# Kernel optimization log

Measured on AMD Instinct MI355X. Metric: run time of the kernel, lower is better.

Reference implementation:

```python
import jax, jax.numpy as jnp
import numpy as np

IN_FEATURES = 4096
OUT_FEATURES = 4096
M_TOKENS = 8192
WEIGHT_SCALE = 0.1
OUT_SCALE = 0.1


def setup_inputs() -> dict:
    key = jax.random.key(0)
    k_x, k_w = jax.random.split(key)
    # int8-valued activations and weights in [-128, 128), stored as int32 carriers
    x_q = jax.random.randint(k_x, (M_TOKENS, IN_FEATURES), 0, 256, dtype=jnp.int32) - 128
    weight_q = jax.random.randint(k_w, (OUT_FEATURES, IN_FEATURES), 0, 256, dtype=jnp.int32) - 128
    scale_x = jnp.float32(0.05)
    return {"x_q": x_q, "weight_q": weight_q, "scale_x": scale_x}


def reference(x_q, weight_q, scale_x):
    acc = jnp.einsum("mk,nk->mn", x_q.astype(jnp.int32), weight_q.astype(jnp.int32))
    # fused epilogue: rescale, round-to-nearest, saturate to int8
    scale = scale_x * jnp.float32(WEIGHT_SCALE) / jnp.float32(OUT_SCALE)
    y = acc.astype(jnp.float32) * scale
    y_q = jnp.clip(jnp.round(y), -128.0, 127.0).astype(jnp.int8)
    return (y_q, jnp.float32(OUT_SCALE))
```

## Files before the change

kernel.cpp:

```cpp
#include <hip/hip_runtime.h>
#include <stdint.h>

typedef int v4i  __attribute__((ext_vector_type(4)));
typedef int v16i __attribute__((ext_vector_type(16)));

#define M_TOK 8192
#define N_OUT 4096
#define K_IN  4096

__device__ __forceinline__ int pack4(int4 a) {
    return (a.x & 255) | ((a.y & 255) << 8) | ((a.z & 255) << 16) | ((a.w & 255) << 24);
}

__global__ __launch_bounds__(256) void pack_both(
    const int4* __restrict__ x, const int4* __restrict__ w,
    int* __restrict__ dA, int* __restrict__ dB, int n4x, int n4w)
{
    int i = blockIdx.x * blockDim.x + threadIdx.x;
    if (i < n4x) {
        dA[i] = pack4(x[i]);
    } else {
        int j = i - n4x;
        if (j < n4w) dB[j] = pack4(w[j]);
    }
}

__global__ __launch_bounds__(256) void gemm_i8_kernel(
    const char* __restrict__ A8,
    const char* __restrict__ B8,
    const float* __restrict__ scale_ptr,
    float* __restrict__ out)
{
    __shared__ alignas(16) char lA[128 * 128];
    __shared__ alignas(16) char lB[128 * 128];

    const int tid  = threadIdx.x;
    const int wave = tid >> 6;
    const int lane = tid & 63;

    const int bm = blockIdx.y * 128;
    const int bn = blockIdx.x * 128;

    const int wm = (wave >> 1) * 64;
    const int wn = (wave & 1) * 64;

    v16i acc[2][2];
#pragma unroll
    for (int i = 0; i < 2; ++i)
#pragma unroll
        for (int j = 0; j < 2; ++j)
#pragma unroll
            for (int r = 0; r < 16; ++r)
                acc[i][j][r] = 0;

    const int srow = lane >> 3;
    const int scol = ((lane & 7) ^ srow) << 4;

    const char* gA[4]; const char* gB[4];
    char* lAp[4]; char* lBp[4];
#pragma unroll
    for (int q = 0; q < 4; ++q) {
        int row0 = wave * 32 + q * 8;
        gA[q] = A8 + (size_t)(bm + row0 + srow) * K_IN + scol;
        gB[q] = B8 + (size_t)(bn + row0 + srow) * K_IN + scol;
        lAp[q] = lA + row0 * 128;
        lBp[q] = lB + row0 * 128;
    }

    const int fm = lane & 31;
    const int fh = lane >> 5;
    const int fsw = fm & 7;

    for (int k0 = 0; k0 < K_IN; k0 += 128) {
#pragma unroll
        for (int q = 0; q < 4; ++q) {
            __builtin_amdgcn_global_load_lds(
                (const __attribute__((address_space(1))) void*)(gA[q] + k0),
                (__attribute__((address_space(3))) void*)lAp[q], 16, 0, 0);
            __builtin_amdgcn_global_load_lds(
                (const __attribute__((address_space(1))) void*)(gB[q] + k0),
                (__attribute__((address_space(3))) void*)lBp[q], 16, 0, 0);
        }

        __syncthreads();

#pragma unroll
        for (int kk = 0; kk < 4; ++kk) {
            const int goff = ((kk * 2 + fh) ^ fsw) << 4;
            v4i af[2], bf[2];
#pragma unroll
            for (int t = 0; t < 2; ++t) {
                af[t] = *(const v4i*)(lA + (wm + t * 32 + fm) * 128 + goff);
                bf[t] = *(const v4i*)(lB + (wn + t * 32 + fm) * 128 + goff);
            }
#pragma unroll
            for (int ti = 0; ti < 2; ++ti)
#pragma unroll
                for (int tj = 0; tj < 2; ++tj)
                    acc[ti][tj] = __builtin_amdgcn_mfma_i32_32x32x32_i8(
                        af[ti], bf[tj], acc[ti][tj], 0, 0, 0);
        }

        __syncthreads();
    }

    const float s     = scale_ptr[0];
    const float scale = (s * 0.1f) / 0.1f;

#pragma unroll
    for (int ti = 0; ti < 2; ++ti) {
#pragma unroll
        for (int tj = 0; tj < 2; ++tj) {
#pragma unroll
            for (int r = 0; r < 16; ++r) {
                int row = bm + wm + ti * 32 + (r & 3) + 8 * (r >> 2) + 4 * fh;
                int col = bn + wn + tj * 32 + fm;
                float y = (float)acc[ti][tj][r] * scale;
                y = rintf(y);
                y = fminf(fmaxf(y, -128.0f), 127.0f);
                out[(size_t)row * N_OUT + col] = y;
            }
        }
    }

    if (bm == 0 && bn == 0 && tid == 0)
        out[(size_t)M_TOK * N_OUT] = 0.1f;
}

extern "C" void kernel_launch(void* const* d_in, const int* in_sizes, int n_in,
                              void* d_out, int out_size, void* d_ws, size_t ws_size,
                              hipStream_t stream)
{
    const int*   x_q     = (const int*)d_in[0];
    const int*   w_q     = (const int*)d_in[1];
    const float* scale_x = (const float*)d_in[2];
    float* out = (float*)d_out;

    char* A8 = (char*)d_ws;
    char* B8 = (char*)d_ws + (size_t)M_TOK * K_IN;

    const int n4x = (M_TOK * K_IN) / 4;
    const int n4w = (N_OUT * K_IN) / 4;

    pack_both<<<(n4x + n4w) / 256, 256, 0, stream>>>(
        (const int4*)x_q, (const int4*)w_q, (int*)A8, (int*)B8, n4x, n4w);

    dim3 grid(N_OUT / 128, M_TOK / 128);
    gemm_i8_kernel<<<grid, 256, 0, stream>>>(A8, B8, scale_x, out);
}
```

Measured before the change: 400.8 us.

## Prepack B in MFMA fragment order and double-buffer A in LDS

The pack kernel now writes the weight matrix pre-arranged in MFMA operand fragment order, so the GEMM loads B fragments straight from global memory into registers and skips LDS for B. A gets two LDS buffers, and the next K-tile of A and B is prefetched while MFMAs run on the current one, with one barrier per stage instead of two. The grid is also transposed so blocks along M are adjacent in launch order. The cost is more registers for the B prefetch buffers, and every wave reads B directly from global or L2 memory without reuse through LDS.

Result: slower. 418.3 us (+4.4%).

```diff
diff --git a/kernel.cpp b/kernel.cpp
--- a/kernel.cpp
+++ b/kernel.cpp
@@ -12,34 +12,46 @@
     return (a.x & 255) | ((a.y & 255) << 8) | ((a.z & 255) << 16) | ((a.w & 255) << 24);
 }
 
-__global__ __launch_bounds__(256) void pack_both(
-    const int4* __restrict__ x, const int4* __restrict__ w,
-    int* __restrict__ dA, int* __restrict__ dB, int n4x, int n4w)
+__global__ __launch_bounds__(256) void pack_kernel(
+    const int4* __restrict__ x, const int* __restrict__ w,
+    int* __restrict__ dA, int4* __restrict__ dBp, int n4x, int nB16)
 {
     int i = blockIdx.x * blockDim.x + threadIdx.x;
     if (i < n4x) {
         dA[i] = pack4(x[i]);
     } else {
-        int j = i - n4x;
-        if (j < n4w) dB[j] = pack4(w[j]);
+        int t = i - n4x;
+        if (t < nB16) {
+            int lane = t & 63;
+            int c    = (t >> 6) & 127;
+            int n32  = t >> 13;
+            int row  = n32 * 32 + (lane & 31);
+            int col  = c * 32 + (lane >> 5) * 16;
+            const int4* src = (const int4*)(w + (size_t)row * K_IN + col);
+            int4 p;
+            p.x = pack4(src[0]);
+            p.y = pack4(src[1]);
+            p.z = pack4(src[2]);
+            p.w = pack4(src[3]);
+            dBp[t] = p;
+        }
     }
 }
 
 __global__ __launch_bounds__(256) void gemm_i8_kernel(
     const char* __restrict__ A8,
-    const char* __restrict__ B8,
+    const int*  __restrict__ Bp,
     const float* __restrict__ scale_ptr,
     float* __restrict__ out)
 {
-    __shared__ alignas(16) char lA[128 * 128];
-    __shared__ alignas(16) char lB[128 * 128];
+    __shared__ alignas(16) char lA[2][128 * 128];
 
     const int tid  = threadIdx.x;
     const int wave = tid >> 6;
     const int lane = tid & 63;
 
-    const int bm = blockIdx.y * 128;
-    const int bn = blockIdx.x * 128;
+    const int bm = blockIdx.x * 128;
+    const int bn = blockIdx.y * 128;
 
     const int wm = (wave >> 1) * 64;
     const int wn = (wave & 1) * 64;
@@ -56,52 +68,89 @@
     const int srow = lane >> 3;
     const int scol = ((lane & 7) ^ srow) << 4;
 
-    const char* gA[4]; const char* gB[4];
-    char* lAp[4]; char* lBp[4];
+    const char* gA[4];
+    char* lp0[4];
+    char* lp1[4];
 #pragma unroll
     for (int q = 0; q < 4; ++q) {
         int row0 = wave * 32 + q * 8;
-        gA[q] = A8 + (size_t)(bm + row0 + srow) * K_IN + scol;
-        gB[q] = B8 + (size_t)(bn + row0 + srow) * K_IN + scol;
-        lAp[q] = lA + row0 * 128;
-        lBp[q] = lB + row0 * 128;
+        gA[q]  = A8 + (size_t)(bm + row0 + srow) * K_IN + scol;
+        lp0[q] = lA[0] + row0 * 128;
+        lp1[q] = lA[1] + row0 * 128;
     }
 
-    const int fm = lane & 31;
-    const int fh = lane >> 5;
+    const v4i* Bb = (const v4i*)Bp + (size_t)((bn >> 5) + (wn >> 5)) * (128 * 64) + lane;
+
+    const int fm  = lane & 31;
+    const int fh  = lane >> 5;
     const int fsw = fm & 7;
 
-    for (int k0 = 0; k0 < K_IN; k0 += 128) {
-#pragma unroll
-        for (int q = 0; q < 4; ++q) {
-            __builtin_amdgcn_global_load_lds(
-                (const __attribute__((address_space(1))) void*)(gA[q] + k0),
-                (__attribute__((address_space(3))) void*)lAp[q], 16, 0, 0);
-            __builtin_amdgcn_global_load_lds(
-                (const __attribute__((address_space(1))) void*)(gB[q] + k0),
-                (__attribute__((address_space(3))) void*)lBp[q], 16, 0, 0);
-        }
-
-        __syncthreads();
+    v4i b0[8], b1[8];
 
 #pragma unroll
-        for (int kk = 0; kk < 4; ++kk) {
-            const int goff = ((kk * 2 + fh) ^ fsw) << 4;
-            v4i af[2], bf[2];
+    for (int t = 0; t < 2; ++t)
 #pragma unroll
-            for (int t = 0; t < 2; ++t) {
-                af[t] = *(const v4i*)(lA + (wm + t * 32 + fm) * 128 + goff);
-                bf[t] = *(const v4i*)(lB + (wn + t * 32 + fm) * 128 + goff);
+        for (int kk = 0; kk < 4; ++kk)
+            b0[t * 4 + kk] = Bb[(size_t)(t * 128 + kk) * 64];
+#pragma unroll
+    for (int q = 0; q < 4; ++q)
+        __builtin_amdgcn_global_load_lds(
+            (const __attribute__((address_space(1))) void*)(gA[q]),
+            (__attribute__((address_space(3))) void*)lp0[q], 16, 0, 0);
+    __syncthreads();
+
+#pragma unroll 1
+    for (int k0 = 0; k0 < K_IN; k0 += 256) {
+        {
+            const int kn = (k0 + 128) & (K_IN - 1);
+            const int cn = kn >> 5;
+#pragma unroll
+            for (int t = 0; t < 2; ++t)
+#pragma unroll
+                for (int kk = 0; kk < 4; ++kk)
+                    b1[t * 4 + kk] = Bb[(size_t)(t * 128 + cn + kk) * 64];
+#pragma unroll
+            for (int q = 0; q < 4; ++q)
+                __builtin_amdgcn_global_load_lds(
+                    (const __attribute__((address_space(1))) void*)(gA[q] + kn),
+                    (__attribute__((address_space(3))) void*)lp1[q], 16, 0, 0);
+#pragma unroll
+            for (int kk = 0; kk < 4; ++kk) {
+                const int goff = ((kk * 2 + fh) ^ fsw) << 4;
+                v4i af0 = *(const v4i*)(lA[0] + (wm + fm) * 128 + goff);
+                v4i af1 = *(const v4i*)(lA[0] + (wm + 32 + fm) * 128 + goff);
+                acc[0][0] = __builtin_amdgcn_mfma_i32_32x32x32_i8(af0, b0[kk],     acc[0][0], 0, 0, 0);
+                acc[0][1] = __builtin_amdgcn_mfma_i32_32x32x32_i8(af0, b0[4 + kk], acc[0][1], 0, 0, 0);
+                acc[1][0] = __builtin_amdgcn_mfma_i32_32x32x32_i8(af1, b0[kk],     acc[1][0], 0, 0, 0);
+                acc[1][1] = __builtin_amdgcn_mfma_i32_32x32x32_i8(af1, b0[4 + kk], acc[1][1], 0, 0, 0);
             }
+            __syncthreads();
+        }
+        {
+            const int kn = (k0 + 256) & (K_IN - 1);
+            const int cn = kn >> 5;
 #pragma unroll
-            for (int ti = 0; ti < 2; ++ti)
+            for (int t = 0; t < 2; ++t)
 #pragma unroll
-                for (int tj = 0; tj < 2; ++tj)
-                    acc[ti][tj] = __builtin_amdgcn_mfma_i32_32x32x32_i8(
-                        af[ti], bf[tj], acc[ti][tj], 0, 0, 0);
+                for (int kk = 0; kk < 4; ++kk)
+                    b0[t * 4 + kk] = Bb[(size_t)(t * 128 + cn + kk) * 64];
+#pragma unroll
+            for (int q = 0; q < 4; ++q)
+                __builtin_amdgcn_global_load_lds(
+                    (const __attribute__((address_space(1))) void*)(gA[q] + kn),
+                    (__attribute__((address_space(3))) void*)lp0[q], 16, 0, 0);
+#pragma unroll
+            for (int kk = 0; kk < 4; ++kk) {
+                const int goff = ((kk * 2 + fh) ^ fsw) << 4;
+                v4i af0 = *(const v4i*)(lA[1] + (wm + fm) * 128 + goff);
+                v4i af1 = *(const v4i*)(lA[1] + (wm + 32 + fm) * 128 + goff);
+                acc[0][0] = __builtin_amdgcn_mfma_i32_32x32x32_i8(af0, b1[kk],     acc[0][0], 0, 0, 0);
+                acc[0][1] = __builtin_amdgcn_mfma_i32_32x32x32_i8(af0, b1[4 + kk], acc[0][1], 0, 0, 0);
+                acc[1][0] = __builtin_amdgcn_mfma_i32_32x32x32_i8(af1, b1[kk],     acc[1][0], 0, 0, 0);
+                acc[1][1] = __builtin_amdgcn_mfma_i32_32x32x32_i8(af1, b1[4 + kk], acc[1][1], 0, 0, 0);
+            }
+            __syncthreads();
         }
-
-        __syncthreads();
     }
 
     const float s     = scale_ptr[0];
@@ -137,14 +186,14 @@
     float* out = (float*)d_out;
 
     char* A8 = (char*)d_ws;
-    char* B8 = (char*)d_ws + (size_t)M_TOK * K_IN;
+    char* Bp = (char*)d_ws + (size_t)M_TOK * K_IN;
 
-    const int n4x = (M_TOK * K_IN) / 4;
-    const int n4w = (N_OUT * K_IN) / 4;
+    const int n4x  = (M_TOK * K_IN) / 4;
+    const int nB16 = (N_OUT * K_IN) / 16;
 
-    pack_both<<<(n4x + n4w) / 256, 256, 0, stream>>>(
-        (const int4*)x_q, (const int4*)w_q, (int*)A8, (int*)B8, n4x, n4w);
+    pack_kernel<<<(n4x + nB16 + 255) / 256, 256, 0, stream>>>(
+        (const int4*)x_q, w_q, (int*)A8, (int4*)Bp, n4x, nB16);
 
-    dim3 grid(N_OUT / 128, M_TOK / 128);
-    gemm_i8_kernel<<<grid, 256, 0, stream>>>(A8, B8, scale_x, out);
+    dim3 grid(M_TOK / 128, N_OUT / 128);
+    gemm_i8_kernel<<<grid, 256, 0, stream>>>(A8, (const int*)Bp, scale_x, out);
 }
```

## Pre-pack int8 operands in MFMA fragment order and load directly to registers

Applied to the files above, without the earlier changes.

The pack kernel now writes A and B in a fragment-major layout that matches what the 32x32x32 i8 MFMA expects per lane. The GEMM then skips LDS and barriers and loads fragments straight from global memory into registers, double-buffered across 128-wide K steps. The grid axes are also swapped so consecutive blocks walk along M. Each wave re-reads its operands from global/L2 with no sharing through LDS, which raises cache traffic and register pressure.

Result: slower. 434.9 us (+8.5%).

```diff
diff --git a/kernel.cpp b/kernel.cpp
--- a/kernel.cpp
+++ b/kernel.cpp
@@ -12,34 +12,44 @@
     return (a.x & 255) | ((a.y & 255) << 8) | ((a.z & 255) << 16) | ((a.w & 255) << 24);
 }
 
-__global__ __launch_bounds__(256) void pack_both(
-    const int4* __restrict__ x, const int4* __restrict__ w,
-    int* __restrict__ dA, int* __restrict__ dB, int n4x, int n4w)
+__device__ __forceinline__ void pack_frag(
+    const int* __restrict__ src, int4* __restrict__ dst, int t)
+{
+    int lane = t & 63;
+    int c    = (t >> 6) & 127;
+    int g32  = t >> 13;
+    int row  = g32 * 32 + (lane & 31);
+    int col  = c * 32 + (lane >> 5) * 16;
+    const int4* s = (const int4*)(src + (size_t)row * K_IN + col);
+    int4 p;
+    p.x = pack4(s[0]);
+    p.y = pack4(s[1]);
+    p.z = pack4(s[2]);
+    p.w = pack4(s[3]);
+    dst[t] = p;
+}
+
+__global__ __launch_bounds__(256) void pack_kernel(
+    const int* __restrict__ x, const int* __restrict__ w,
+    int4* __restrict__ dAp, int4* __restrict__ dBp, int nA16, int nB16)
 {
     int i = blockIdx.x * blockDim.x + threadIdx.x;
-    if (i < n4x) {
-        dA[i] = pack4(x[i]);
-    } else {
-        int j = i - n4x;
-        if (j < n4w) dB[j] = pack4(w[j]);
-    }
+    if (i < nA16)             pack_frag(x, dAp, i);
+    else if (i - nA16 < nB16) pack_frag(w, dBp, i - nA16);
 }
 
 __global__ __launch_bounds__(256) void gemm_i8_kernel(
-    const char* __restrict__ A8,
-    const char* __restrict__ B8,
+    const int* __restrict__ Ap,
+    const int* __restrict__ Bp,
     const float* __restrict__ scale_ptr,
     float* __restrict__ out)
 {
-    __shared__ alignas(16) char lA[128 * 128];
-    __shared__ alignas(16) char lB[128 * 128];
-
     const int tid  = threadIdx.x;
     const int wave = tid >> 6;
     const int lane = tid & 63;
 
-    const int bm = blockIdx.y * 128;
-    const int bn = blockIdx.x * 128;
+    const int bm = blockIdx.x * 128;
+    const int bn = blockIdx.y * 128;
 
     const int wm = (wave >> 1) * 64;
     const int wn = (wave & 1) * 64;
@@ -53,59 +63,61 @@
             for (int r = 0; r < 16; ++r)
                 acc[i][j][r] = 0;
 
-    const int srow = lane >> 3;
-    const int scol = ((lane & 7) ^ srow) << 4;
+    const v4i* Ab = (const v4i*)Ap + (size_t)((bm + wm) >> 5) * (128 * 64) + lane;
+    const v4i* Bb = (const v4i*)Bp + (size_t)((bn + wn) >> 5) * (128 * 64) + lane;
 
-    const char* gA[4]; const char* gB[4];
-    char* lAp[4]; char* lBp[4];
+    v4i a0[8], b0[8], a1[8], b1[8];
+
 #pragma unroll
-    for (int q = 0; q < 4; ++q) {
-        int row0 = wave * 32 + q * 8;
-        gA[q] = A8 + (size_t)(bm + row0 + srow) * K_IN + scol;
-        gB[q] = B8 + (size_t)(bn + row0 + srow) * K_IN + scol;
-        lAp[q] = lA + row0 * 128;
-        lBp[q] = lB + row0 * 128;
-    }
-
-    const int fm = lane & 31;
-    const int fh = lane >> 5;
-    const int fsw = fm & 7;
-
-    for (int k0 = 0; k0 < K_IN; k0 += 128) {
+    for (int t = 0; t < 2; ++t)
 #pragma unroll
-        for (int q = 0; q < 4; ++q) {
-            __builtin_amdgcn_global_load_lds(
-                (const __attribute__((address_space(1))) void*)(gA[q] + k0),
-                (__attribute__((address_space(3))) void*)lAp[q], 16, 0, 0);
-            __builtin_amdgcn_global_load_lds(
-                (const __attribute__((address_space(1))) void*)(gB[q] + k0),
-                (__attribute__((address_space(3))) void*)lBp[q], 16, 0, 0);
+        for (int kk = 0; kk < 4; ++kk) {
+            a0[t * 4 + kk] = Ab[(size_t)(t * 128 + kk) * 64];
+            b0[t * 4 + kk] = Bb[(size_t)(t * 128 + kk) * 64];
         }
 
-        __syncthreads();
-
+#pragma unroll 1
+    for (int k0 = 0; k0 < K_IN; k0 += 256) {
+        {
+            const int cn = (((k0 + 128) & (K_IN - 1)) >> 5);
 #pragma unroll
-        for (int kk = 0; kk < 4; ++kk) {
-            const int goff = ((kk * 2 + fh) ^ fsw) << 4;
-            v4i af[2], bf[2];
+            for (int t = 0; t < 2; ++t)
 #pragma unroll
-            for (int t = 0; t < 2; ++t) {
-                af[t] = *(const v4i*)(lA + (wm + t * 32 + fm) * 128 + goff);
-                bf[t] = *(const v4i*)(lB + (wn + t * 32 + fm) * 128 + goff);
+                for (int kk = 0; kk < 4; ++kk) {
+                    a1[t * 4 + kk] = Ab[(size_t)(t * 128 + cn + kk) * 64];
+                    b1[t * 4 + kk] = Bb[(size_t)(t * 128 + cn + kk) * 64];
+                }
+#pragma unroll
+            for (int kk = 0; kk < 4; ++kk) {
+                acc[0][0] = __builtin_amdgcn_mfma_i32_32x32x32_i8(a0[kk],     b0[kk],     acc[0][0], 0, 0, 0);
+                acc[0][1] = __builtin_amdgcn_mfma_i32_32x32x32_i8(a0[kk],     b0[4 + kk], acc[0][1], 0, 0, 0);
+                acc[1][0] = __builtin_amdgcn_mfma_i32_32x32x32_i8(a0[4 + kk], b0[kk],     acc[1][0], 0, 0, 0);
+                acc[1][1] = __builtin_amdgcn_mfma_i32_32x32x32_i8(a0[4 + kk], b0[4 + kk], acc[1][1], 0, 0, 0);
             }
+        }
+        {
+            const int cn = (((k0 + 256) & (K_IN - 1)) >> 5);
 #pragma unroll
-            for (int ti = 0; ti < 2; ++ti)
+            for (int t = 0; t < 2; ++t)
 #pragma unroll
-                for (int tj = 0; tj < 2; ++tj)
-                    acc[ti][tj] = __builtin_amdgcn_mfma_i32_32x32x32_i8(
-                        af[ti], bf[tj], acc[ti][tj], 0, 0, 0);
+                for (int kk = 0; kk < 4; ++kk) {
+                    a0[t * 4 + kk] = Ab[(size_t)(t * 128 + cn + kk) * 64];
+                    b0[t * 4 + kk] = Bb[(size_t)(t * 128 + cn + kk) * 64];
+                }
+#pragma unroll
+            for (int kk = 0; kk < 4; ++kk) {
+                acc[0][0] = __builtin_amdgcn_mfma_i32_32x32x32_i8(a1[kk],     b1[kk],     acc[0][0], 0, 0, 0);
+                acc[0][1] = __builtin_amdgcn_mfma_i32_32x32x32_i8(a1[kk],     b1[4 + kk], acc[0][1], 0, 0, 0);
+                acc[1][0] = __builtin_amdgcn_mfma_i32_32x32x32_i8(a1[4 + kk], b1[kk],     acc[1][0], 0, 0, 0);
+                acc[1][1] = __builtin_amdgcn_mfma_i32_32x32x32_i8(a1[4 + kk], b1[4 + kk], acc[1][1], 0, 0, 0);
+            }
         }
-
-        __syncthreads();
     }
 
     const float s     = scale_ptr[0];
     const float scale = (s * 0.1f) / 0.1f;
+    const int fm = lane & 31;
+    const int fh = lane >> 5;
 
 #pragma unroll
     for (int ti = 0; ti < 2; ++ti) {
@@ -136,15 +148,16 @@
     const float* scale_x = (const float*)d_in[2];
     float* out = (float*)d_out;
 
-    char* A8 = (char*)d_ws;
-    char* B8 = (char*)d_ws + (size_t)M_TOK * K_IN;
+    char* Ap = (char*)d_ws;
+    char* Bp = (char*)d_ws + (size_t)M_TOK * K_IN;
 
-    const int n4x = (M_TOK * K_IN) / 4;
-    const int n4w = (N_OUT * K_IN) / 4;
+    const int nA16 = (M_TOK * K_IN) / 16;
+    const int nB16 = (N_OUT * K_IN) / 16;
 
-    pack_both<<<(n4x + n4w) / 256, 256, 0, stream>>>(
-        (const int4*)x_q, (const int4*)w_q, (int*)A8, (int*)B8, n4x, n4w);
+    pack_kernel<<<(nA16 + nB16) / 256, 256, 0, stream>>>(
+        x_q, w_q, (int4*)Ap, (int4*)Bp, nA16, nB16);
 
-    dim3 grid(N_OUT / 128, M_TOK / 128);
-    gemm_i8_kernel<<<grid, 256, 0, stream>>>(A8, B8, scale_x, out);
+    dim3 grid(M_TOK / 128, N_OUT / 128);
+    gemm_i8_kernel<<<grid, 256, 0, stream>>>(
+        (const int*)Ap, (const int*)Bp, scale_x, out);
 }
```

## Double-buffer LDS tiles to overlap global loads with MFMA compute

Applied to the files above, without the earlier changes.

Splits the A and B shared-memory tiles into two buffers and prefetches the next K-slab with global_load_lds while MFMAs run on the current one. This is meant to hide global-to-LDS latency that the single-buffer load, sync, compute, sync loop exposed. LDS use doubles to 64KB per block, which may cut occupancy. The sync placement also relies on the async LDS loads completing at the barrier.

New measurement: 416.3 us. +3.9%, slower.

```diff
diff --git a/kernel.cpp b/kernel.cpp
--- a/kernel.cpp
+++ b/kernel.cpp
@@ -31,8 +31,8 @@
     const float* __restrict__ scale_ptr,
     float* __restrict__ out)
 {
-    __shared__ alignas(16) char lA[128 * 128];
-    __shared__ alignas(16) char lB[128 * 128];
+    __shared__ alignas(16) char lA[2][128 * 128];
+    __shared__ alignas(16) char lB[2][128 * 128];
 
     const int tid  = threadIdx.x;
     const int wave = tid >> 6;
@@ -57,52 +57,66 @@
     const int scol = ((lane & 7) ^ srow) << 4;
 
     const char* gA[4]; const char* gB[4];
-    char* lAp[4]; char* lBp[4];
+    char* lAp[2][4]; char* lBp[2][4];
 #pragma unroll
     for (int q = 0; q < 4; ++q) {
         int row0 = wave * 32 + q * 8;
         gA[q] = A8 + (size_t)(bm + row0 + srow) * K_IN + scol;
         gB[q] = B8 + (size_t)(bn + row0 + srow) * K_IN + scol;
-        lAp[q] = lA + row0 * 128;
-        lBp[q] = lB + row0 * 128;
+        lAp[0][q] = lA[0] + row0 * 128;
+        lAp[1][q] = lA[1] + row0 * 128;
+        lBp[0][q] = lB[0] + row0 * 128;
+        lBp[1][q] = lB[1] + row0 * 128;
     }
 
-    const int fm = lane & 31;
-    const int fh = lane >> 5;
+    const int fm  = lane & 31;
+    const int fh  = lane >> 5;
     const int fsw = fm & 7;
 
-    for (int k0 = 0; k0 < K_IN; k0 += 128) {
-#pragma unroll
-        for (int q = 0; q < 4; ++q) {
-            __builtin_amdgcn_global_load_lds(
-                (const __attribute__((address_space(1))) void*)(gA[q] + k0),
-                (__attribute__((address_space(3))) void*)lAp[q], 16, 0, 0);
-            __builtin_amdgcn_global_load_lds(
-                (const __attribute__((address_space(1))) void*)(gB[q] + k0),
-                (__attribute__((address_space(3))) void*)lBp[q], 16, 0, 0);
-        }
+#define STAGE(koff, buf)                                                      \
+    {                                                                         \
+        _Pragma("unroll")                                                     \
+        for (int q = 0; q < 4; ++q) {                                         \
+            __builtin_amdgcn_global_load_lds(                                 \
+                (const __attribute__((address_space(1))) void*)(gA[q] + (koff)), \
+                (__attribute__((address_space(3))) void*)lAp[buf][q], 16, 0, 0); \
+            __builtin_amdgcn_global_load_lds(                                 \
+                (const __attribute__((address_space(1))) void*)(gB[q] + (koff)), \
+                (__attribute__((address_space(3))) void*)lBp[buf][q], 16, 0, 0); \
+        }                                                                     \
+    }
 
+#define COMPUTE(buf)                                                          \
+    {                                                                         \
+        _Pragma("unroll")                                                     \
+        for (int kk = 0; kk < 4; ++kk) {                                      \
+            const int goff = ((kk * 2 + fh) ^ fsw) << 4;                      \
+            v4i af0 = *(const v4i*)(lA[buf] + (wm + fm) * 128 + goff);        \
+            v4i af1 = *(const v4i*)(lA[buf] + (wm + 32 + fm) * 128 + goff);   \
+            v4i bf0 = *(const v4i*)(lB[buf] + (wn + fm) * 128 + goff);        \
+            v4i bf1 = *(const v4i*)(lB[buf] + (wn + 32 + fm) * 128 + goff);   \
+            acc[0][0] = __builtin_amdgcn_mfma_i32_32x32x32_i8(af0, bf0, acc[0][0], 0, 0, 0); \
+            acc[0][1] = __builtin_amdgcn_mfma_i32_32x32x32_i8(af0, bf1, acc[0][1], 0, 0, 0); \
+            acc[1][0] = __builtin_amdgcn_mfma_i32_32x32x32_i8(af1, bf0, acc[1][0], 0, 0, 0); \
+            acc[1][1] = __builtin_amdgcn_mfma_i32_32x32x32_i8(af1, bf1, acc[1][1], 0, 0, 0); \
+        }                                                                     \
+    }
+
+    STAGE(0, 0);
+    __syncthreads();
+
+#pragma unroll 1
+    for (int k0 = 0; k0 < K_IN; k0 += 256) {
+        if (k0 + 128 < K_IN) STAGE(k0 + 128, 1);
+        COMPUTE(0);
         __syncthreads();
-
-#pragma unroll
-        for (int kk = 0; kk < 4; ++kk) {
-            const int goff = ((kk * 2 + fh) ^ fsw) << 4;
-            v4i af[2], bf[2];
-#pragma unroll
-            for (int t = 0; t < 2; ++t) {
-                af[t] = *(const v4i*)(lA + (wm + t * 32 + fm) * 128 + goff);
-                bf[t] = *(const v4i*)(lB + (wn + t * 32 + fm) * 128 + goff);
-            }
-#pragma unroll
-            for (int ti = 0; ti < 2; ++ti)
-#pragma unroll
-                for (int tj = 0; tj < 2; ++tj)
-                    acc[ti][tj] = __builtin_amdgcn_mfma_i32_32x32x32_i8(
-                        af[ti], bf[tj], acc[ti][tj], 0, 0, 0);
-        }
-
+        if (k0 + 256 < K_IN) STAGE(k0 + 256, 0);
+        COMPUTE(1);
         __syncthreads();
     }
+
+#undef STAGE
+#undef COMPUTE
 
     const float s     = scale_ptr[0];
     const float scale = (s * 0.1f) / 0.1f;
```
